# Kernel optimization log

Measured on AMD Instinct MI355X. Metric: run time of the kernel, lower is better.

The kernel has to match this reference:

```python
import jax, jax.numpy as jnp
import numpy as np

B, C, D_IN, D_H, D_OUT = 131072, 16, 256, 1024, 256


def setup_inputs() -> dict:
    key = jax.random.key(0)
    k = jax.random.split(key, 6)
    return {
        "x": jax.random.normal(k[0], (B, D_IN), dtype=jnp.float32),
        "cat_ids": jax.random.randint(k[1], (B,), 0, C, dtype=jnp.int32),
        "W1": jax.random.normal(k[2], (C, D_IN, D_H), dtype=jnp.float32) * (1.0 / np.sqrt(D_IN)),
        "b1": jax.random.normal(k[3], (C, D_H), dtype=jnp.float32) * 0.02,
        "W2": jax.random.normal(k[4], (C, D_H, D_OUT), dtype=jnp.float32) * (1.0 / np.sqrt(D_H)),
        "b2": jax.random.normal(k[5], (C, D_OUT), dtype=jnp.float32) * 0.02,
    }


def _routed_linear(x, cat_ids, W, b):
    # Category-routed linear: out[i] = x[i] @ W[cat_ids[i]] + b[cat_ids[i]].
    # Loop over the small fixed category count (not over tokens); each branch
    # is a dense GEMM masked by the routing assignment. This is equivalent to
    # the original gather -> per-category Linear -> scatter/argsort pattern
    # without materializing per-token weight gathers.
    num_categories = W.shape[0]
    out = jnp.zeros((x.shape[0], W.shape[2]), dtype=x.dtype)
    for c in range(num_categories):
        mask = (cat_ids == c)[:, None]
        out = out + jnp.where(mask, x @ W[c] + b[c], jnp.zeros((), x.dtype))
    return out


def reference(x, cat_ids, W1, b1, W2, b2):
    hidden = jax.nn.relu(_routed_linear(x, cat_ids, W1, b1))
    return _routed_linear(hidden, cat_ids, W2, b2)
```

## Files before the change

### kernel.cpp

```cpp
#include <hip/hip_runtime.h>
#include <hip/hip_bf16.h>

#define BB   131072
#define CC   16
#define DIN  256
#define DH   1024
#define DOUT 256
#define TM   128
#define NB   512

typedef __attribute__((ext_vector_type(8))) short bf16x8;
typedef __attribute__((ext_vector_type(4))) short short4v;
typedef __attribute__((ext_vector_type(4))) float f32x4;
typedef __attribute__((ext_vector_type(4))) float float4v;

__device__ inline unsigned short f2b(float f) {
  union { float f; unsigned u; } v; v.f = f;
  unsigned u = v.u;
  return (unsigned short)((u + 0x7fffu + ((u >> 16) & 1u)) >> 16);
}

__device__ inline void gload_lds16(const void* g, void* l) {
  __builtin_amdgcn_global_load_lds(
      (const __attribute__((address_space(1))) void*)g,
      (__attribute__((address_space(3))) void*)l, 16, 0, 0);
}

#define MFMA16(a, b, c) __builtin_amdgcn_mfma_f32_16x16x32_bf16((a), (b), (c), 0, 0, 0)

__global__ void hist_k(const int* __restrict__ cat, int* __restrict__ blockhist) {
  __shared__ int h[CC];
  const int tid = threadIdx.x;
  if (tid < CC) h[tid] = 0;
  __syncthreads();
  const int i = blockIdx.x * 256 + tid;
  atomicAdd(&h[cat[i]], 1);
  __syncthreads();
  if (tid < CC) blockhist[blockIdx.x * CC + tid] = h[tid];
}

__global__ void offsets2_k(const int* __restrict__ blockhist,
                           int* __restrict__ counts, int* __restrict__ padoff,
                           int* __restrict__ base) {
  __shared__ int part[CC][64];
  __shared__ int pref[CC][64];
  __shared__ int scnt[CC];
  __shared__ int spad[CC + 1];
  const int tid = threadIdx.x;
  const int c = tid >> 6;
  const int g = tid & 63;
  int h[8];
  int s = 0;
#pragma unroll
  for (int i = 0; i < 8; i++) {
    h[i] = blockhist[(g * 8 + i) * CC + c];
    s += h[i];
  }
  part[c][g] = s;
  __syncthreads();
  if (g == 0) {
    int r = 0;
    for (int j = 0; j < 64; j++) { pref[c][j] = r; r += part[c][j]; }
    scnt[c] = r;
  }
  __syncthreads();
  if (tid == 0) {
    int acc = 0;
    for (int c2 = 0; c2 < CC; c2++) {
      spad[c2] = acc;
      padoff[c2] = acc;
      counts[c2] = scnt[c2];
      acc += ((scnt[c2] + TM - 1) / TM) * TM;
    }
    spad[CC] = acc;
    padoff[CC] = acc;
  }
  __syncthreads();
  int run = spad[c] + pref[c][g];
#pragma unroll
  for (int i = 0; i < 8; i++) {
    base[(g * 8 + i) * CC + c] = run;
    run += h[i];
  }
}

__global__ void scatter2_k(const int* __restrict__ cat, const int* __restrict__ base,
                           int* __restrict__ idx) {
  __shared__ int cur[CC];
  const int tid = threadIdx.x;
  if (tid < CC) cur[tid] = base[blockIdx.x * CC + tid];
  __syncthreads();
  const int i = blockIdx.x * 256 + tid;
  const int c = cat[i];
  const int pos = atomicAdd(&cur[c], 1);
  idx[pos] = i;
}

__global__ void conv_w1_k(const float* __restrict__ W1, short* __restrict__ w1b) {
  int t = blockIdx.x * blockDim.x + threadIdx.x;
  int n = t & 1023;
  int j = (t >> 10) & 31;
  int c = t >> 15;
  const float* src = W1 + (size_t)c * 256 * 1024;
  bf16x8 o;
#pragma unroll
  for (int i = 0; i < 8; i++)
    o[i] = (short)f2b(src[(size_t)(j * 8 + i) * 1024 + n]);
  char* dst = (char*)w1b + (size_t)(c * 1024 + n) * 512 + ((j * 16) ^ ((n & 7) << 4));
  *(bf16x8*)dst = o;
}

__global__ void conv_w2_k(const float* __restrict__ W2, short* __restrict__ w2b) {
  int t = blockIdx.x * blockDim.x + threadIdx.x;
  int n = t & 255;
  int j = (t >> 8) & 127;
  int c = t >> 15;
  const float* src = W2 + (size_t)c * 1024 * 256;
  bf16x8 o;
#pragma unroll
  for (int i = 0; i < 8; i++)
    o[i] = (short)f2b(src[(size_t)(j * 8 + i) * 256 + n]);
  char* dst = (char*)w2b + (size_t)(c * 256 + n) * 2048 + ((j * 16) ^ ((n & 7) << 4));
  *(bf16x8*)dst = o;
}

#define W2OFF  65536
#define HSOFF  131072
#define TKOFF  147456
#define B1OFF  147968
#define B2OFF  152064

__launch_bounds__(512, 2)
__global__ void mlp_k(const float* __restrict__ x,
                      const float* __restrict__ b1,
                      const float* __restrict__ b2,
                      const short* __restrict__ w1b,
                      const short* __restrict__ w2b,
                      const int* __restrict__ idx,
                      const int* __restrict__ padoff,
                      const int* __restrict__ counts,
                      float* __restrict__ out) {
  __shared__ __align__(16) char sm[153088];

  const int bhw = blockIdx.x;
  const int wg = (bhw & 7) * 130 + (bhw >> 3);
  const int p = wg * TM;
  const int total = padoff[CC];
  if (p >= total) return;
  int c = 0;
  while (padoff[c + 1] <= p) c++;
  const int cnt = counts[c];
  const int start = p - padoff[c];

  const int tid  = threadIdx.x;
  const int lane = tid & 63;
  const int w    = tid >> 6;
  const int wt   = w & 3;
  const int wh   = w >> 2;
  const int lrow = lane & 15;
  const int lgrp = lane >> 4;

  char* hsb   = sm + HSOFF;
  int*  toksp = (int*)(sm + TKOFF);
  float* b1s  = (float*)(sm + B1OFF);
  float* b2s  = (float*)(sm + B2OFF);

  {
    const int r = tid >> 2;
    const int q = tid & 3;
    const int pos = start + r;
    int tok = -1;
    if (pos < cnt) tok = idx[p + r];
    if (q == 0) toksp[r] = tok;
    const int swz = (r & 7) << 4;
    char* rowbase = sm + r * 512;
    if (tok >= 0) {
      const float4v* src = (const float4v*)(x + (size_t)tok * DIN) + q * 16;
#pragma unroll
      for (int j = 0; j < 8; j++) {
        float4v v0 = src[2 * j];
        float4v v1 = src[2 * j + 1];
        bf16x8 o;
        o[0] = (short)f2b(v0[0]); o[1] = (short)f2b(v0[1]);
        o[2] = (short)f2b(v0[2]); o[3] = (short)f2b(v0[3]);
        o[4] = (short)f2b(v1[0]); o[5] = (short)f2b(v1[1]);
        o[6] = (short)f2b(v1[2]); o[7] = (short)f2b(v1[3]);
        *(bf16x8*)(rowbase + ((q * 128 + j * 16) ^ swz)) = o;
      }
    } else {
      bf16x8 z = {0, 0, 0, 0, 0, 0, 0, 0};
#pragma unroll
      for (int j = 0; j < 8; j++)
        *(bf16x8*)(rowbase + ((q * 128 + j * 16) ^ swz)) = z;
    }
    if (tid < 256) ((f32x4*)b1s)[tid] = ((const f32x4*)(b1 + (size_t)c * DH))[tid];
    if (tid < 64)  ((f32x4*)b2s)[tid] = ((const f32x4*)(b2 + (size_t)c * DOUT))[tid];
  }
  __syncthreads();

  bf16x8 xf[2][8];
#pragma unroll
  for (int ti = 0; ti < 2; ti++) {
    const int r = wt * 32 + ti * 16 + lrow;
    const int swz = (r & 7) << 4;
#pragma unroll
    for (int ks = 0; ks < 8; ks++)
      xf[ti][ks] = *(const bf16x8*)(sm + r * 512 + ((ks * 64 + lgrp * 16) ^ swz));
  }
  __syncthreads();

  const char* w1g = (const char*)w1b + (size_t)c * 1024 * 512;
  const char* w2g = (const char*)w2b + (size_t)c * 256 * 2048;

  auto stage1 = [&](int i) {
    const char* src = w1g + (size_t)i * 32768;
    char* dst = sm + (i & 1) * 32768;
#pragma unroll
    for (int j = 0; j < 4; j++) {
      int chunk = (w * 4 + j) * 1024;
      gload_lds16(src + chunk + lane * 16, dst + chunk);
    }
  };
  auto stage2 = [&](int i) {
    char* dst = sm + W2OFF + (i & 1) * 32768;
#pragma unroll
    for (int j = 0; j < 4; j++) {
      int o = (w * 4 + j) * 1024 + lane * 16;
      int n = o >> 7;
      int q = o & 127;
      gload_lds16(w2g + (size_t)n * 2048 + i * 128 + q, dst + (w * 4 + j) * 1024);
    }
  };

  stage1(0);
  stage2(0);
  __syncthreads();

  f32x4 acc2[8][2];
#pragma unroll
  for (int ni = 0; ni < 8; ni++)
#pragma unroll
    for (int ti = 0; ti < 2; ti++)
      acc2[ni][ti] = (f32x4){0.f, 0.f, 0.f, 0.f};

  for (int hb = 0; hb < 16; hb++) {
    const char* w1c = sm + (hb & 1) * 32768;
    const char* w2c = sm + W2OFF + (hb & 1) * 32768;

    f32x4 acc1[2][2];
#pragma unroll
    for (int ni = 0; ni < 2; ni++)
#pragma unroll
      for (int ti = 0; ti < 2; ti++)
        acc1[ni][ti] = (f32x4){0.f, 0.f, 0.f, 0.f};

#pragma unroll
    for (int ks = 0; ks < 8; ks++) {
      bf16x8 a1[2];
#pragma unroll
      for (int ni = 0; ni < 2; ni++) {
        int n = wh * 32 + ni * 16 + lrow;
        a1[ni] = *(const bf16x8*)(w1c + n * 512 + ((ks * 64 + lgrp * 16) ^ ((n & 7) << 4)));
      }
#pragma unroll
      for (int ni = 0; ni < 2; ni++)
#pragma unroll
        for (int ti = 0; ti < 2; ti++)
          acc1[ni][ti] = MFMA16(a1[ni], xf[ti][ks], acc1[ni][ti]);
    }

#pragma unroll
    for (int ni = 0; ni < 2; ni++) {
      const int n0 = wh * 32 + ni * 16 + lgrp * 4;
      f32x4 bv = *(const f32x4*)(b1s + hb * 64 + n0);
#pragma unroll
      for (int ti = 0; ti < 2; ti++) {
        const int r = wt * 32 + ti * 16 + lrow;
        short4v h;
#pragma unroll
        for (int jj = 0; jj < 4; jj++) {
          float v = fmaxf(acc1[ni][ti][jj] + bv[jj], 0.0f);
          h[jj] = (short)f2b(v);
        }
        *(short4v*)(hsb + r * 128 + ((n0 * 2) ^ ((r & 7) << 4))) = h;
      }
    }
    asm volatile("s_waitcnt vmcnt(0) lgkmcnt(0)" ::: "memory");
    __builtin_amdgcn_s_barrier();

    if (hb < 15) { stage1(hb + 1); stage2(hb + 1); }

#pragma unroll
    for (int ks = 0; ks < 2; ks++) {
      bf16x8 bh[2];
#pragma unroll
      for (int ti = 0; ti < 2; ti++) {
        int r = wt * 32 + ti * 16 + lrow;
        bh[ti] = *(const bf16x8*)(hsb + r * 128 + ((ks * 64 + lgrp * 16) ^ ((r & 7) << 4)));
      }
#pragma unroll
      for (int ni = 0; ni < 8; ni++) {
        int n = wh * 128 + ni * 16 + lrow;
        bf16x8 a2 = *(const bf16x8*)(w2c + n * 128 + ((ks * 64 + lgrp * 16) ^ ((n & 7) << 4)));
#pragma unroll
        for (int ti = 0; ti < 2; ti++)
          acc2[ni][ti] = MFMA16(a2, bh[ti], acc2[ni][ti]);
      }
    }
    asm volatile("s_waitcnt vmcnt(4) lgkmcnt(0)" ::: "memory");
    __builtin_amdgcn_s_barrier();
  }

#pragma unroll
  for (int ni = 0; ni < 8; ni++) {
    const int n0 = wh * 128 + ni * 16 + lgrp * 4;
    f32x4 bv = *(const f32x4*)(b2s + n0);
#pragma unroll
    for (int ti = 0; ti < 2; ti++) {
      const int rr = wt * 32 + ti * 16 + lrow;
      const int tok = toksp[rr];
      if (tok >= 0) {
        f32x4 v = acc2[ni][ti] + bv;
        *(f32x4*)(out + (size_t)tok * DOUT + n0) = v;
      }
    }
  }
}

extern "C" void kernel_launch(void* const* d_in, const int* in_sizes, int n_in,
                              void* d_out, int out_size, void* d_ws, size_t ws_size,
                              hipStream_t stream) {
  (void)in_sizes; (void)n_in; (void)out_size; (void)ws_size;
  const float* x   = (const float*)d_in[0];
  const int*   cat = (const int*)d_in[1];
  const float* W1  = (const float*)d_in[2];
  const float* b1  = (const float*)d_in[3];
  const float* W2  = (const float*)d_in[4];
  const float* b2  = (const float*)d_in[5];
  float* out = (float*)d_out;

  char* ws = (char*)d_ws;
  int* counts    = (int*)(ws);
  int* padoff    = (int*)(ws + 128);
  int* blockhist = (int*)(ws + 4096);
  int* base      = (int*)(ws + 65536);
  int* idx       = (int*)(ws + 131072);
  short* w1b     = (short*)(ws + (1 << 20));
  short* w2b     = (short*)(ws + (1 << 20) + 8388608);

  hist_k<<<NB, 256, 0, stream>>>(cat, blockhist);
  offsets2_k<<<1, 1024, 0, stream>>>(blockhist, counts, padoff, base);
  scatter2_k<<<NB, 256, 0, stream>>>(cat, base, idx);
  conv_w1_k<<<2048, 256, 0, stream>>>(W1, w1b);
  conv_w2_k<<<2048, 256, 0, stream>>>(W2, w2b);

  const int ntiles = BB / TM + CC;
  mlp_k<<<ntiles, 512, 0, stream>>>(x, b1, b2, w1b, w2b, idx, padoff, counts, out);
}
```

Measured before the change: 267.4 us.

## Halve token tile to 64 and hidden chunk to 32 for higher occupancy

Shrinks the per-workgroup token tile from 128 to 64 rows and the hidden chunk per iteration from 64 to 32, halving LDS use so four workgroups can reside per CU instead of two. The wave layout changes to 4x2, so each wave now handles one 16-row token tile, which shrinks register use. The W2 staging swizzle is dropped because rows are now 64 bytes. In exchange, each weight byte loaded is reused across fewer tokens, doubling weight traffic from L2. Barriers per hidden dimension double, and unswizzled W2 reads may hit LDS bank conflicts.

```diff
diff --git a/kernel.cpp b/kernel.cpp
--- a/kernel.cpp
+++ b/kernel.cpp
@@ -6,7 +6,8 @@
 #define DIN  256
 #define DH   1024
 #define DOUT 256
-#define TM   128
+#define TM   64
+#define NHB  32
 #define NB   512
 
 typedef __attribute__((ext_vector_type(8))) short bf16x8;
@@ -120,17 +121,18 @@
 #pragma unroll
   for (int i = 0; i < 8; i++)
     o[i] = (short)f2b(src[(size_t)(j * 8 + i) * 256 + n]);
-  char* dst = (char*)w2b + (size_t)(c * 256 + n) * 2048 + ((j * 16) ^ ((n & 7) << 4));
+  char* dst = (char*)w2b + (size_t)(c * 256 + n) * 2048 + j * 16;
   *(bf16x8*)dst = o;
 }
 
-#define W2OFF  65536
-#define HSOFF  131072
-#define TKOFF  147456
-#define B1OFF  147968
-#define B2OFF  152064
-
-__launch_bounds__(512, 2)
+#define W2OFF  32768
+#define HSOFF  65536
+#define TKOFF  69632
+#define B1OFF  69888
+#define B2OFF  73984
+#define SMSZ   75008
+
+__launch_bounds__(512, 4)
 __global__ void mlp_k(const float* __restrict__ x,
                       const float* __restrict__ b1,
                       const float* __restrict__ b2,
@@ -140,10 +142,10 @@
                       const int* __restrict__ padoff,
                       const int* __restrict__ counts,
                       float* __restrict__ out) {
-  __shared__ __align__(16) char sm[153088];
+  __shared__ __align__(16) char sm[SMSZ];
 
   const int bhw = blockIdx.x;
-  const int wg = (bhw & 7) * 130 + (bhw >> 3);
+  const int wg = (bhw & 7) * 258 + (bhw >> 3);
   const int p = wg * TM;
   const int total = padoff[CC];
   if (p >= total) return;
@@ -155,57 +157,55 @@
   const int tid  = threadIdx.x;
   const int lane = tid & 63;
   const int w    = tid >> 6;
-  const int wt   = w & 3;
-  const int wh   = w >> 2;
+  const int wt   = w >> 1;
+  const int wh   = w & 1;
   const int lrow = lane & 15;
   const int lgrp = lane >> 4;
 
-  char* hsb   = sm + HSOFF;
-  int*  toksp = (int*)(sm + TKOFF);
-  float* b1s  = (float*)(sm + B1OFF);
-  float* b2s  = (float*)(sm + B2OFF);
+  char*  hsb   = sm + HSOFF;
+  int*   toksp = (int*)(sm + TKOFF);
+  float* b1s   = (float*)(sm + B1OFF);
+  float* b2s   = (float*)(sm + B2OFF);
 
   {
-    const int r = tid >> 2;
-    const int q = tid & 3;
+    const int r = tid >> 3;
+    const int q = tid & 7;
     const int pos = start + r;
-    int tok = -1;
-    if (pos < cnt) tok = idx[p + r];
+    int tok = (pos < cnt) ? idx[p + r] : -1;
     if (q == 0) toksp[r] = tok;
     const int swz = (r & 7) << 4;
-    char* rowbase = sm + r * 512;
+    char* rowb = sm + r * 512;
     if (tok >= 0) {
-      const float4v* src = (const float4v*)(x + (size_t)tok * DIN) + q * 16;
-#pragma unroll
-      for (int j = 0; j < 8; j++) {
-        float4v v0 = src[2 * j];
-        float4v v1 = src[2 * j + 1];
+      const float4v* src = (const float4v*)(x + (size_t)tok * DIN) + q * 8;
+#pragma unroll
+      for (int m = 0; m < 4; m++) {
+        float4v v0 = src[2 * m];
+        float4v v1 = src[2 * m + 1];
         bf16x8 o;
         o[0] = (short)f2b(v0[0]); o[1] = (short)f2b(v0[1]);
         o[2] = (short)f2b(v0[2]); o[3] = (short)f2b(v0[3]);
         o[4] = (short)f2b(v1[0]); o[5] = (short)f2b(v1[1]);
         o[6] = (short)f2b(v1[2]); o[7] = (short)f2b(v1[3]);
-        *(bf16x8*)(rowbase + ((q * 128 + j * 16) ^ swz)) = o;
+        *(bf16x8*)(rowb + ((q * 64 + m * 16) ^ swz)) = o;
       }
     } else {
       bf16x8 z = {0, 0, 0, 0, 0, 0, 0, 0};
 #pragma unroll
-      for (int j = 0; j < 8; j++)
-        *(bf16x8*)(rowbase + ((q * 128 + j * 16) ^ swz)) = z;
+      for (int m = 0; m < 4; m++)
+        *(bf16x8*)(rowb + ((q * 64 + m * 16) ^ swz)) = z;
     }
     if (tid < 256) ((f32x4*)b1s)[tid] = ((const f32x4*)(b1 + (size_t)c * DH))[tid];
     if (tid < 64)  ((f32x4*)b2s)[tid] = ((const f32x4*)(b2 + (size_t)c * DOUT))[tid];
   }
   __syncthreads();
 
-  bf16x8 xf[2][8];
-#pragma unroll
-  for (int ti = 0; ti < 2; ti++) {
-    const int r = wt * 32 + ti * 16 + lrow;
+  bf16x8 xf[8];
+  {
+    const int r = wt * 16 + lrow;
     const int swz = (r & 7) << 4;
 #pragma unroll
     for (int ks = 0; ks < 8; ks++)
-      xf[ti][ks] = *(const bf16x8*)(sm + r * 512 + ((ks * 64 + lgrp * 16) ^ swz));
+      xf[ks] = *(const bf16x8*)(sm + r * 512 + ((ks * 64 + lgrp * 16) ^ swz));
   }
   __syncthreads();
 
@@ -213,116 +213,82 @@
   const char* w2g = (const char*)w2b + (size_t)c * 256 * 2048;
 
   auto stage1 = [&](int i) {
-    const char* src = w1g + (size_t)i * 32768;
-    char* dst = sm + (i & 1) * 32768;
-#pragma unroll
-    for (int j = 0; j < 4; j++) {
-      int chunk = (w * 4 + j) * 1024;
+    const char* src = w1g + (size_t)i * 16384;
+    char* dst = sm + (i & 1) * 16384;
+#pragma unroll
+    for (int j = 0; j < 2; j++) {
+      int chunk = (w * 2 + j) * 1024;
       gload_lds16(src + chunk + lane * 16, dst + chunk);
     }
   };
   auto stage2 = [&](int i) {
-    char* dst = sm + W2OFF + (i & 1) * 32768;
-#pragma unroll
-    for (int j = 0; j < 4; j++) {
-      int o = (w * 4 + j) * 1024 + lane * 16;
-      int n = o >> 7;
-      int q = o & 127;
-      gload_lds16(w2g + (size_t)n * 2048 + i * 128 + q, dst + (w * 4 + j) * 1024);
+    char* dst = sm + W2OFF + (i & 1) * 16384;
+#pragma unroll
+    for (int j = 0; j < 2; j++) {
+      int o = (w * 2 + j) * 1024 + lane * 16;
+      int n = o >> 6;
+      int q = o & 63;
+      gload_lds16(w2g + (size_t)n * 2048 + i * 64 + q, dst + (w * 2 + j) * 1024);
     }
   };
 
   stage1(0);
   stage2(0);
-  __syncthreads();
-
-  f32x4 acc2[8][2];
+  asm volatile("s_waitcnt vmcnt(0)" ::: "memory");
+  __syncthreads();
+
+  f32x4 acc2[8];
 #pragma unroll
   for (int ni = 0; ni < 8; ni++)
-#pragma unroll
-    for (int ti = 0; ti < 2; ti++)
-      acc2[ni][ti] = (f32x4){0.f, 0.f, 0.f, 0.f};
-
-  for (int hb = 0; hb < 16; hb++) {
-    const char* w1c = sm + (hb & 1) * 32768;
-    const char* w2c = sm + W2OFF + (hb & 1) * 32768;
-
-    f32x4 acc1[2][2];
-#pragma unroll
-    for (int ni = 0; ni < 2; ni++)
-#pragma unroll
-      for (int ti = 0; ti < 2; ti++)
-        acc1[ni][ti] = (f32x4){0.f, 0.f, 0.f, 0.f};
-
+    acc2[ni] = (f32x4){0.f, 0.f, 0.f, 0.f};
+
+  const int rtok = wt * 16 + lrow;
+
+  for (int hb = 0; hb < NHB; hb++) {
+    const char* w1c = sm + (hb & 1) * 16384;
+    const char* w2c = sm + W2OFF + (hb & 1) * 16384;
+
+    f32x4 acc1 = (f32x4){0.f, 0.f, 0.f, 0.f};
+    const int n1 = wh * 16 + lrow;
+    const int sw1 = (n1 & 7) << 4;
 #pragma unroll
     for (int ks = 0; ks < 8; ks++) {
-      bf16x8 a1[2];
-#pragma unroll
-      for (int ni = 0; ni < 2; ni++) {
-        int n = wh * 32 + ni * 16 + lrow;
-        a1[ni] = *(const bf16x8*)(w1c + n * 512 + ((ks * 64 + lgrp * 16) ^ ((n & 7) << 4)));
-      }
-#pragma unroll
-      for (int ni = 0; ni < 2; ni++)
-#pragma unroll
-        for (int ti = 0; ti < 2; ti++)
-          acc1[ni][ti] = MFMA16(a1[ni], xf[ti][ks], acc1[ni][ti]);
-    }
-
-#pragma unroll
-    for (int ni = 0; ni < 2; ni++) {
-      const int n0 = wh * 32 + ni * 16 + lgrp * 4;
-      f32x4 bv = *(const f32x4*)(b1s + hb * 64 + n0);
-#pragma unroll
-      for (int ti = 0; ti < 2; ti++) {
-        const int r = wt * 32 + ti * 16 + lrow;
-        short4v h;
-#pragma unroll
-        for (int jj = 0; jj < 4; jj++) {
-          float v = fmaxf(acc1[ni][ti][jj] + bv[jj], 0.0f);
-          h[jj] = (short)f2b(v);
-        }
-        *(short4v*)(hsb + r * 128 + ((n0 * 2) ^ ((r & 7) << 4))) = h;
-      }
+      bf16x8 a1 = *(const bf16x8*)(w1c + n1 * 512 + ((ks * 64 + lgrp * 16) ^ sw1));
+      acc1 = MFMA16(a1, xf[ks], acc1);
+    }
+    {
+      const int n0 = wh * 16 + lgrp * 4;
+      f32x4 bv = *(const f32x4*)(b1s + hb * 32 + n0);
+      short4v h;
+#pragma unroll
+      for (int jj = 0; jj < 4; jj++)
+        h[jj] = (short)f2b(fmaxf(acc1[jj] + bv[jj], 0.0f));
+      *(short4v*)(hsb + rtok * 64 + wh * 32 + lgrp * 8) = h;
     }
     asm volatile("s_waitcnt vmcnt(0) lgkmcnt(0)" ::: "memory");
     __builtin_amdgcn_s_barrier();
 
-    if (hb < 15) { stage1(hb + 1); stage2(hb + 1); }
-
-#pragma unroll
-    for (int ks = 0; ks < 2; ks++) {
-      bf16x8 bh[2];
-#pragma unroll
-      for (int ti = 0; ti < 2; ti++) {
-        int r = wt * 32 + ti * 16 + lrow;
-        bh[ti] = *(const bf16x8*)(hsb + r * 128 + ((ks * 64 + lgrp * 16) ^ ((r & 7) << 4)));
-      }
-#pragma unroll
-      for (int ni = 0; ni < 8; ni++) {
-        int n = wh * 128 + ni * 16 + lrow;
-        bf16x8 a2 = *(const bf16x8*)(w2c + n * 128 + ((ks * 64 + lgrp * 16) ^ ((n & 7) << 4)));
-#pragma unroll
-        for (int ti = 0; ti < 2; ti++)
-          acc2[ni][ti] = MFMA16(a2, bh[ti], acc2[ni][ti]);
-      }
-    }
-    asm volatile("s_waitcnt vmcnt(4) lgkmcnt(0)" ::: "memory");
+    if (hb < NHB - 1) { stage1(hb + 1); stage2(hb + 1); }
+
+    bf16x8 hf = *(const bf16x8*)(hsb + rtok * 64 + lgrp * 16);
+#pragma unroll
+    for (int ni = 0; ni < 8; ni++) {
+      const int n = wh * 128 + ni * 16 + lrow;
+      bf16x8 a2 = *(const bf16x8*)(w2c + n * 64 + lgrp * 16);
+      acc2[ni] = MFMA16(a2, hf, acc2[ni]);
+    }
+    asm volatile("s_waitcnt vmcnt(2) lgkmcnt(0)" ::: "memory");
     __builtin_amdgcn_s_barrier();
   }
 
-#pragma unroll
-  for (int ni = 0; ni < 8; ni++) {
-    const int n0 = wh * 128 + ni * 16 + lgrp * 4;
-    f32x4 bv = *(const f32x4*)(b2s + n0);
-#pragma unroll
-    for (int ti = 0; ti < 2; ti++) {
-      const int rr = wt * 32 + ti * 16 + lrow;
-      const int tok = toksp[rr];
-      if (tok >= 0) {
-        f32x4 v = acc2[ni][ti] + bv;
-        *(f32x4*)(out + (size_t)tok * DOUT + n0) = v;
-      }
+  const int tok = toksp[rtok];
+  if (tok >= 0) {
+#pragma unroll
+    for (int ni = 0; ni < 8; ni++) {
+      const int n0 = wh * 128 + ni * 16 + lgrp * 4;
+      f32x4 bv = *(const f32x4*)(b2s + n0);
+      f32x4 v = acc2[ni] + bv;
+      *(f32x4*)(out + (size_t)tok * DOUT + n0) = v;
     }
   }
 }
```

Result: slower. 292.9 us (+9.5%).
